# Performance work log

Measured on AMD Instinct MI355X. Metric: run time of the kernel, lower is better.

## Reference

```python
import jax, jax.numpy as jnp
import numpy as np


def setup_inputs() -> dict:
    key = jax.random.key(0)
    k1, k2 = jax.random.split(key)
    pred = jax.random.normal(k1, (1, 2048, 512), dtype=jnp.float32)
    cand = jax.random.normal(k2, (1, 65536, 512), dtype=jnp.float32)
    return {
        "predicted_transaction_company": pred,
        "future_transaction_companies_inc_current_data": cand,
    }


def reference(predicted_transaction_company, future_transaction_companies_inc_current_data):
    # torch.cdist with p=2 on [1,P,D] x [1,R,D] -> [1,P,R]; squeeze(0) -> [P,R]; global min.
    x = predicted_transaction_company[0]                       # [P, D]
    y = future_transaction_companies_inc_current_data[0]       # [R, D]
    sq = (
        jnp.sum(x * x, axis=-1)[:, None]
        + jnp.sum(y * y, axis=-1)[None, :]
        - 2.0 * jnp.einsum("pd,rd->pr", x, y)
    )                                                          # [P, R]
    distances = jnp.sqrt(jnp.maximum(sq, 0.0))
    return jnp.min(distances)
```

## Files before the change

kernel.cpp:

```cpp
#include <hip/hip_runtime.h>
#include <stdint.h>

#define P 2048
#define R 65536
#define DD 512
#define BM 256
#define BN 256
#define BK 64
#define NT (DD / BK)

typedef __attribute__((ext_vector_type(8))) short short8;
typedef __attribute__((ext_vector_type(4))) float f32x4;

__device__ inline unsigned short f2bf(float f) {
  unsigned int u = __float_as_uint(f);
  u += 0x7fffu + ((u >> 16) & 1u);
  return (unsigned short)(u >> 16);
}

__device__ inline void gload_lds16(const void* g, void* l) {
  __builtin_amdgcn_global_load_lds(
      (const __attribute__((address_space(1))) unsigned int*)g,
      (__attribute__((address_space(3))) unsigned int*)l,
      16, 0, 0);
}

__global__ __launch_bounds__(256) void k_convert(
    const float* __restrict__ pred, const float* __restrict__ cand,
    unsigned short* __restrict__ Abf, unsigned short* __restrict__ Bbf,
    float* __restrict__ nx, float* __restrict__ ny,
    unsigned int* __restrict__ minp)
{
  if (blockIdx.x == 0 && threadIdx.x == 0) *minp = 0x7f800000u;
  const int lane = threadIdx.x & 63;
  const int wv   = (blockIdx.x << 2) | (threadIdx.x >> 6);
  const int nw   = gridDim.x << 2;
  for (int gw = wv; gw < P + R; gw += nw) {
    const float* src; unsigned short* dst; float* np;
    if (gw < P) { src = pred + (size_t)gw * DD; dst = Abf + (size_t)gw * DD; np = nx + gw; }
    else { int r = gw - P; src = cand + (size_t)r * DD; dst = Bbf + (size_t)r * DD; np = ny + r; }
    const float4* s4 = ((const float4*)src) + lane * 2;
    float4 v0 = s4[0], v1 = s4[1];
    float ss = v0.x*v0.x + v0.y*v0.y + v0.z*v0.z + v0.w*v0.w
             + v1.x*v1.x + v1.y*v1.y + v1.z*v1.z + v1.w*v1.w;
    union { unsigned short h[8]; uint4 v; } pk;
    pk.h[0]=f2bf(v0.x); pk.h[1]=f2bf(v0.y); pk.h[2]=f2bf(v0.z); pk.h[3]=f2bf(v0.w);
    pk.h[4]=f2bf(v1.x); pk.h[5]=f2bf(v1.y); pk.h[6]=f2bf(v1.z); pk.h[7]=f2bf(v1.w);
    *(uint4*)(dst + (size_t)lane * 8) = pk.v;
    #pragma unroll
    for (int off = 32; off; off >>= 1) ss += __shfl_down(ss, off, 64);
    if (lane == 0) *np = ss;
  }
}

__global__ __launch_bounds__(512, 2) void k_gemm_min(
    const unsigned short* __restrict__ Abf, const unsigned short* __restrict__ Bbf,
    const float* __restrict__ nx, const float* __restrict__ ny,
    unsigned int* __restrict__ minp)
{
  __shared__ __align__(16) unsigned short As[2][BM * BK];
  __shared__ __align__(16) unsigned short Bs[2][BN * BK];
  __shared__ float wmin[8];

  const int tid  = threadIdx.x;
  const int wave = tid >> 6;
  const int lane = tid & 63;

  const int raw = blockIdx.x;
  const int wg  = (raw & 7) * 256 + (raw >> 3);
  const int by  = wg & 7;
  const int bx  = wg >> 3;
  const int rowA0 = by * BM, rowB0 = bx * BN;
  const int wr = wave >> 2;
  const int wc = wave & 3;

  f32x4 zero = {0.f, 0.f, 0.f, 0.f};
  f32x4 acc[8][4];
  #pragma unroll
  for (int i = 0; i < 8; ++i)
    #pragma unroll
    for (int j = 0; j < 4; ++j) acc[i][j] = zero;

  const int rloc = lane >> 3;
  const int cswz = (lane & 7) ^ rloc;
  const unsigned short* gA[4]; const unsigned short* gB[4];
  int lofs[4];
  #pragma unroll
  for (int t = 0; t < 4; ++t) {
    const int ii = wave * 4 + t;
    gA[t] = Abf + (size_t)(rowA0 + ii * 8 + rloc) * DD + cswz * 8;
    gB[t] = Bbf + (size_t)(rowB0 + ii * 8 + rloc) * DD + cswz * 8;
    lofs[t] = ii * 512;
  }

#define STAGE(s, kt) do { const int _k0 = (kt) * BK;            \
    _Pragma("unroll")                                           \
    for (int _t = 0; _t < 4; ++_t) {                            \
      gload_lds16(gA[_t] + _k0, &As[s][lofs[_t]]);              \
      gload_lds16(gB[_t] + _k0, &Bs[s][lofs[_t]]);              \
    } } while (0)

  const int m = lane & 15, quad = lane >> 4, mb = m & 7;
  const int aRow0 = (wr * 128 + m) * BK;
  const int bRow0 = (wc * 64  + m) * BK;
  const int swz0 = ((quad    ) ^ mb) * 8;
  const int swz1 = ((quad + 4) ^ mb) * 8;

  STAGE(0, 0);

  #pragma unroll 2
  for (int T = 0; T < NT; ++T) {
    const int s = T & 1;
    if (T + 1 < NT) {
      STAGE(s ^ 1, T + 1);
      asm volatile("s_waitcnt vmcnt(8)" ::: "memory");
    } else {
      asm volatile("s_waitcnt vmcnt(0)" ::: "memory");
    }
    __builtin_amdgcn_s_barrier();
    __builtin_amdgcn_sched_barrier(0);

    const unsigned short* A0 = &As[s][0];
    const unsigned short* B0 = &Bs[s][0];
    short8 af[4][2], b0[2][2], b1[2][2];

    #pragma unroll
    for (int i = 0; i < 4; ++i) {
      const unsigned short* ap = A0 + aRow0 + i * 16 * BK;
      af[i][0] = *(const short8*)(ap + swz0);
      af[i][1] = *(const short8*)(ap + swz1);
    }
    #pragma unroll
    for (int j = 0; j < 2; ++j) {
      const unsigned short* bp = B0 + bRow0 + j * 16 * BK;
      b0[j][0] = *(const short8*)(bp + swz0);
      b0[j][1] = *(const short8*)(bp + swz1);
    }
    #pragma unroll
    for (int j = 0; j < 2; ++j) {
      const unsigned short* bp = B0 + bRow0 + (2 + j) * 16 * BK;
      b1[j][0] = *(const short8*)(bp + swz0);
      b1[j][1] = *(const short8*)(bp + swz1);
    }
    asm volatile("s_waitcnt lgkmcnt(4)" ::: "memory");
    __builtin_amdgcn_sched_barrier(0);
    __builtin_amdgcn_s_setprio(1);
    #pragma unroll
    for (int i = 0; i < 4; ++i)
      #pragma unroll
      for (int j = 0; j < 2; ++j) {
        acc[i][j] = __builtin_amdgcn_mfma_f32_16x16x32_bf16(af[i][0], b0[j][0], acc[i][j], 0, 0, 0);
        acc[i][j] = __builtin_amdgcn_mfma_f32_16x16x32_bf16(af[i][1], b0[j][1], acc[i][j], 0, 0, 0);
      }
    __builtin_amdgcn_s_setprio(0);
    asm volatile("s_waitcnt lgkmcnt(0)" ::: "memory");
    __builtin_amdgcn_sched_barrier(0);
    __builtin_amdgcn_s_setprio(1);
    #pragma unroll
    for (int i = 0; i < 4; ++i)
      #pragma unroll
      for (int j = 0; j < 2; ++j) {
        acc[i][2 + j] = __builtin_amdgcn_mfma_f32_16x16x32_bf16(af[i][0], b1[j][0], acc[i][2 + j], 0, 0, 0);
        acc[i][2 + j] = __builtin_amdgcn_mfma_f32_16x16x32_bf16(af[i][1], b1[j][1], acc[i][2 + j], 0, 0, 0);
      }
    __builtin_amdgcn_s_setprio(0);

    #pragma unroll
    for (int i = 0; i < 4; ++i) {
      const unsigned short* ap = A0 + aRow0 + (4 + i) * 16 * BK;
      af[i][0] = *(const short8*)(ap + swz0);
      af[i][1] = *(const short8*)(ap + swz1);
    }
    asm volatile("s_waitcnt lgkmcnt(0)" ::: "memory");
    __builtin_amdgcn_sched_barrier(0);
    __builtin_amdgcn_s_setprio(1);
    #pragma unroll
    for (int i = 0; i < 4; ++i) {
      #pragma unroll
      for (int j = 0; j < 2; ++j) {
        acc[4 + i][j]     = __builtin_amdgcn_mfma_f32_16x16x32_bf16(af[i][0], b0[j][0], acc[4 + i][j], 0, 0, 0);
        acc[4 + i][j]     = __builtin_amdgcn_mfma_f32_16x16x32_bf16(af[i][1], b0[j][1], acc[4 + i][j], 0, 0, 0);
      }
      #pragma unroll
      for (int j = 0; j < 2; ++j) {
        acc[4 + i][2 + j] = __builtin_amdgcn_mfma_f32_16x16x32_bf16(af[i][0], b1[j][0], acc[4 + i][2 + j], 0, 0, 0);
        acc[4 + i][2 + j] = __builtin_amdgcn_mfma_f32_16x16x32_bf16(af[i][1], b1[j][1], acc[4 + i][2 + j], 0, 0, 0);
      }
    }
    __builtin_amdgcn_s_setprio(0);
    __builtin_amdgcn_s_barrier();
  }
#undef STAGE

  float lmin = 3.4e38f;
  #pragma unroll
  for (int i = 0; i < 8; ++i) {
    const int mbase = rowA0 + wr * 128 + i * 16 + quad * 4;
    float4 nxv = *(const float4*)(nx + mbase);
    #pragma unroll
    for (int j = 0; j < 4; ++j) {
      const int n = rowB0 + wc * 64 + j * 16 + m;
      const float nyv = ny[n];
      f32x4 a = acc[i][j];
      lmin = fminf(lmin, nxv.x + nyv - 2.0f * a[0]);
      lmin = fminf(lmin, nxv.y + nyv - 2.0f * a[1]);
      lmin = fminf(lmin, nxv.z + nyv - 2.0f * a[2]);
      lmin = fminf(lmin, nxv.w + nyv - 2.0f * a[3]);
    }
  }
  #pragma unroll
  for (int off = 32; off; off >>= 1) lmin = fminf(lmin, __shfl_down(lmin, off, 64));
  if (lane == 0) wmin[wave] = lmin;
  __syncthreads();
  if (tid == 0) {
    float mn = wmin[0];
    #pragma unroll
    for (int w = 1; w < 8; ++w) mn = fminf(mn, wmin[w]);
    atomicMin(minp, __float_as_uint(fmaxf(mn, 0.0f)));
  }
}

__global__ __launch_bounds__(64) void k_initmin(unsigned int* minp) {
  if (threadIdx.x == 0) *minp = 0x7f800000u;
}

__global__ __launch_bounds__(256) void k_brute(
    const float* __restrict__ pred, const float* __restrict__ cand,
    unsigned int* __restrict__ minp)
{
  __shared__ float yrow[DD];
  __shared__ float wm[4];
  const int c = blockIdx.x;
  for (int i = threadIdx.x; i < DD; i += 256) yrow[i] = cand[(size_t)c * DD + i];
  __syncthreads();
  float lmin = 3.4e38f;
  for (int p = threadIdx.x; p < P; p += 256) {
    const float* xp = pred + (size_t)p * DD;
    float s = 0.f;
    for (int k = 0; k < DD; ++k) { float d = xp[k] - yrow[k]; s = fmaf(d, d, s); }
    lmin = fminf(lmin, s);
  }
  #pragma unroll
  for (int off = 32; off; off >>= 1) lmin = fminf(lmin, __shfl_down(lmin, off, 64));
  if ((threadIdx.x & 63) == 0) wm[threadIdx.x >> 6] = lmin;
  __syncthreads();
  if (threadIdx.x == 0) {
    float mn = fminf(fminf(wm[0], wm[1]), fminf(wm[2], wm[3]));
    atomicMin(minp, __float_as_uint(fmaxf(mn, 0.0f)));
  }
}

__global__ __launch_bounds__(64) void k_finalize(const unsigned int* minp, float* out) {
  if (threadIdx.x == 0) out[0] = sqrtf(__uint_as_float(*minp));
}

extern "C" void kernel_launch(void* const* d_in, const int* in_sizes, int n_in,
                              void* d_out, int out_size, void* d_ws, size_t ws_size,
                              hipStream_t stream) {
  const float* pred = (const float*)d_in[0];
  const float* cand = (const float*)d_in[1];
  float* out = (float*)d_out;

  unsigned int* minp = (unsigned int*)d_ws;
  float* wsf = (float*)d_ws;
  float* nx = wsf + 16;
  float* ny = nx + P;
  unsigned short* Abf = (unsigned short*)(ny + R);
  unsigned short* Bbf = Abf + (size_t)P * DD;
  const size_t need = (size_t)(16 + P + R) * 4 + ((size_t)P * DD + (size_t)R * DD) * 2;

  if (ws_size >= need) {
    k_convert<<<2048, 256, 0, stream>>>(pred, cand, Abf, Bbf, nx, ny, minp);
    k_gemm_min<<<(P / BM) * (R / BN), 512, 0, stream>>>(Abf, Bbf, nx, ny, minp);
  } else {
    k_initmin<<<1, 64, 0, stream>>>(minp);
    k_brute<<<R, 256, 0, stream>>>(pred, cand, minp);
  }
  k_finalize<<<1, 64, 0, stream>>>(minp, out);
}
```

Measured before the change: 348.0 us.

## Switch GEMM inner loop to 32x32x16 bf16 MFMA with pipelined LDS reads

Replaces the 16x16x32 MFMA tiling (8x4 f32x4 accumulators) with 32x32x16 MFMA (4x2 f32x16 accumulators) per wave. LDS fragment reads are split into four k-substeps and double-buffered in registers (aX/aY), so ds_reads overlap the MFMA batches. The goal is fewer fragment loads per FLOP and higher MFMA throughput per instruction. The epilogue is remapped to the 32x32 output layout, which carries a risk of layout or swizzle mistakes.

```diff
diff --git a/kernel.cpp b/kernel.cpp
--- a/kernel.cpp
+++ b/kernel.cpp
@@ -11,6 +11,7 @@
 
 typedef __attribute__((ext_vector_type(8))) short short8;
 typedef __attribute__((ext_vector_type(4))) float f32x4;
+typedef __attribute__((ext_vector_type(16))) float f32x16;
 
 __device__ inline unsigned short f2bf(float f) {
   unsigned int u = __float_as_uint(f);
@@ -74,12 +75,13 @@
   const int wr = wave >> 2;
   const int wc = wave & 3;
 
-  f32x4 zero = {0.f, 0.f, 0.f, 0.f};
-  f32x4 acc[8][4];
-  #pragma unroll
-  for (int i = 0; i < 8; ++i)
-    #pragma unroll
-    for (int j = 0; j < 4; ++j) acc[i][j] = zero;
+  f32x16 acc[4][2];
+  #pragma unroll
+  for (int i = 0; i < 4; ++i)
+    #pragma unroll
+    for (int j = 0; j < 2; ++j)
+      #pragma unroll
+      for (int r = 0; r < 16; ++r) acc[i][j][r] = 0.f;
 
   const int rloc = lane >> 3;
   const int cswz = (lane & 7) ^ rloc;
@@ -100,11 +102,32 @@
       gload_lds16(gB[_t] + _k0, &Bs[s][lofs[_t]]);              \
     } } while (0)
 
-  const int m = lane & 15, quad = lane >> 4, mb = m & 7;
-  const int aRow0 = (wr * 128 + m) * BK;
-  const int bRow0 = (wc * 64  + m) * BK;
-  const int swz0 = ((quad    ) ^ mb) * 8;
-  const int swz1 = ((quad + 4) ^ mb) * 8;
+  const int col31 = lane & 31, h = lane >> 5;
+  const int aBase0 = (wr * 128 + col31) * BK;
+  const int bBase0 = (wc * 64  + col31) * BK;
+  int swks[4];
+  #pragma unroll
+  for (int ks = 0; ks < 4; ++ks) swks[ks] = ((ks * 2 + h) ^ (lane & 7)) * 8;
+
+#define READ(aR, bR, s, ks) do {                                              \
+    _Pragma("unroll")                                                         \
+    for (int _i = 0; _i < 4; ++_i)                                            \
+      aR[_i] = *(const short8*)(&As[s][aBase0 + _i * 32 * BK + swks[ks]]);    \
+    _Pragma("unroll")                                                         \
+    for (int _j = 0; _j < 2; ++_j)                                            \
+      bR[_j] = *(const short8*)(&Bs[s][bBase0 + _j * 32 * BK + swks[ks]]);    \
+  } while (0)
+
+#define MFMA8(aR, bR) do {                                                    \
+    __builtin_amdgcn_s_setprio(1);                                            \
+    _Pragma("unroll")                                                         \
+    for (int _i = 0; _i < 4; ++_i)                                            \
+      _Pragma("unroll")                                                       \
+      for (int _j = 0; _j < 2; ++_j)                                          \
+        acc[_i][_j] = __builtin_amdgcn_mfma_f32_32x32x16_bf16(                \
+            aR[_i], bR[_j], acc[_i][_j], 0, 0, 0);                            \
+    __builtin_amdgcn_s_setprio(0);                                            \
+  } while (0)
 
   STAGE(0, 0);
 
@@ -120,92 +143,45 @@
     __builtin_amdgcn_s_barrier();
     __builtin_amdgcn_sched_barrier(0);
 
-    const unsigned short* A0 = &As[s][0];
-    const unsigned short* B0 = &Bs[s][0];
-    short8 af[4][2], b0[2][2], b1[2][2];
-
-    #pragma unroll
-    for (int i = 0; i < 4; ++i) {
-      const unsigned short* ap = A0 + aRow0 + i * 16 * BK;
-      af[i][0] = *(const short8*)(ap + swz0);
-      af[i][1] = *(const short8*)(ap + swz1);
-    }
-    #pragma unroll
-    for (int j = 0; j < 2; ++j) {
-      const unsigned short* bp = B0 + bRow0 + j * 16 * BK;
-      b0[j][0] = *(const short8*)(bp + swz0);
-      b0[j][1] = *(const short8*)(bp + swz1);
-    }
-    #pragma unroll
-    for (int j = 0; j < 2; ++j) {
-      const unsigned short* bp = B0 + bRow0 + (2 + j) * 16 * BK;
-      b1[j][0] = *(const short8*)(bp + swz0);
-      b1[j][1] = *(const short8*)(bp + swz1);
-    }
-    asm volatile("s_waitcnt lgkmcnt(4)" ::: "memory");
-    __builtin_amdgcn_sched_barrier(0);
-    __builtin_amdgcn_s_setprio(1);
-    #pragma unroll
-    for (int i = 0; i < 4; ++i)
+    short8 aX[4], bX[2], aY[4], bY[2];
+    READ(aX, bX, s, 0);
+    READ(aY, bY, s, 1);
+    asm volatile("s_waitcnt lgkmcnt(6)" ::: "memory");
+    __builtin_amdgcn_sched_barrier(0);
+    MFMA8(aX, bX);
+    READ(aX, bX, s, 2);
+    asm volatile("s_waitcnt lgkmcnt(6)" ::: "memory");
+    __builtin_amdgcn_sched_barrier(0);
+    MFMA8(aY, bY);
+    READ(aY, bY, s, 3);
+    asm volatile("s_waitcnt lgkmcnt(6)" ::: "memory");
+    __builtin_amdgcn_sched_barrier(0);
+    MFMA8(aX, bX);
+    asm volatile("s_waitcnt lgkmcnt(0)" ::: "memory");
+    __builtin_amdgcn_sched_barrier(0);
+    MFMA8(aY, bY);
+    __builtin_amdgcn_s_barrier();
+  }
+#undef STAGE
+#undef READ
+#undef MFMA8
+
+  float lmin = 3.4e38f;
+  #pragma unroll
+  for (int i = 0; i < 4; ++i) {
+    #pragma unroll
+    for (int rq = 0; rq < 4; ++rq) {
+      const int mbase = rowA0 + wr * 128 + i * 32 + rq * 8 + h * 4;
+      float4 nxv = *(const float4*)(nx + mbase);
       #pragma unroll
       for (int j = 0; j < 2; ++j) {
-        acc[i][j] = __builtin_amdgcn_mfma_f32_16x16x32_bf16(af[i][0], b0[j][0], acc[i][j], 0, 0, 0);
-        acc[i][j] = __builtin_amdgcn_mfma_f32_16x16x32_bf16(af[i][1], b0[j][1], acc[i][j], 0, 0, 0);
+        const int n = rowB0 + wc * 64 + j * 32 + col31;
+        const float nyv = ny[n];
+        lmin = fminf(lmin, nxv.x + nyv - 2.0f * acc[i][j][rq * 4 + 0]);
+        lmin = fminf(lmin, nxv.y + nyv - 2.0f * acc[i][j][rq * 4 + 1]);
+        lmin = fminf(lmin, nxv.z + nyv - 2.0f * acc[i][j][rq * 4 + 2]);
+        lmin = fminf(lmin, nxv.w + nyv - 2.0f * acc[i][j][rq * 4 + 3]);
       }
-    __builtin_amdgcn_s_setprio(0);
-    asm volatile("s_waitcnt lgkmcnt(0)" ::: "memory");
-    __builtin_amdgcn_sched_barrier(0);
-    __builtin_amdgcn_s_setprio(1);
-    #pragma unroll
-    for (int i = 0; i < 4; ++i)
-      #pragma unroll
-      for (int j = 0; j < 2; ++j) {
-        acc[i][2 + j] = __builtin_amdgcn_mfma_f32_16x16x32_bf16(af[i][0], b1[j][0], acc[i][2 + j], 0, 0, 0);
-        acc[i][2 + j] = __builtin_amdgcn_mfma_f32_16x16x32_bf16(af[i][1], b1[j][1], acc[i][2 + j], 0, 0, 0);
-      }
-    __builtin_amdgcn_s_setprio(0);
-
-    #pragma unroll
-    for (int i = 0; i < 4; ++i) {
-      const unsigned short* ap = A0 + aRow0 + (4 + i) * 16 * BK;
-      af[i][0] = *(const short8*)(ap + swz0);
-      af[i][1] = *(const short8*)(ap + swz1);
-    }
-    asm volatile("s_waitcnt lgkmcnt(0)" ::: "memory");
-    __builtin_amdgcn_sched_barrier(0);
-    __builtin_amdgcn_s_setprio(1);
-    #pragma unroll
-    for (int i = 0; i < 4; ++i) {
-      #pragma unroll
-      for (int j = 0; j < 2; ++j) {
-        acc[4 + i][j]     = __builtin_amdgcn_mfma_f32_16x16x32_bf16(af[i][0], b0[j][0], acc[4 + i][j], 0, 0, 0);
-        acc[4 + i][j]     = __builtin_amdgcn_mfma_f32_16x16x32_bf16(af[i][1], b0[j][1], acc[4 + i][j], 0, 0, 0);
-      }
-      #pragma unroll
-      for (int j = 0; j < 2; ++j) {
-        acc[4 + i][2 + j] = __builtin_amdgcn_mfma_f32_16x16x32_bf16(af[i][0], b1[j][0], acc[4 + i][2 + j], 0, 0, 0);
-        acc[4 + i][2 + j] = __builtin_amdgcn_mfma_f32_16x16x32_bf16(af[i][1], b1[j][1], acc[4 + i][2 + j], 0, 0, 0);
-      }
-    }
-    __builtin_amdgcn_s_setprio(0);
-    __builtin_amdgcn_s_barrier();
-  }
-#undef STAGE
-
-  float lmin = 3.4e38f;
-  #pragma unroll
-  for (int i = 0; i < 8; ++i) {
-    const int mbase = rowA0 + wr * 128 + i * 16 + quad * 4;
-    float4 nxv = *(const float4*)(nx + mbase);
-    #pragma unroll
-    for (int j = 0; j < 4; ++j) {
-      const int n = rowB0 + wc * 64 + j * 16 + m;
-      const float nyv = ny[n];
-      f32x4 a = acc[i][j];
-      lmin = fminf(lmin, nxv.x + nyv - 2.0f * a[0]);
-      lmin = fminf(lmin, nxv.y + nyv - 2.0f * a[1]);
-      lmin = fminf(lmin, nxv.z + nyv - 2.0f * a[2]);
-      lmin = fminf(lmin, nxv.w + nyv - 2.0f * a[3]);
     }
   }
   #pragma unroll
```

Result: no change. 347.8 us (-0.0%).
